# Kernel tuning notes

Measured on AMD Instinct MI355X. Metric: run time of the kernel, lower is better.

Reference implementation:

```python
import jax, jax.numpy as jnp
import numpy as np

B, T, S, C = 4096, 128, 16, 128
NEG = -1e30  # finite stand-in for -inf to keep grads NaN-free


def setup_inputs() -> dict:
    key = jax.random.key(0)
    k1, k2 = jax.random.split(key)
    prediction = jax.random.normal(k1, (B, T, C), dtype=jnp.float32)  # treated as log-probs, as in the original
    lable = jax.random.normal(k2, (B, S, C), dtype=jnp.float32)       # one-hot-ish label scores
    return {"prediction": prediction, "lable": lable}


def _ctc_nll(logp, targets):
    """CTC negative log-likelihood, full-length inputs/targets.
    logp: (B, T, C) log-probabilities, blank=0. targets: (B, S) int.
    Returns nll: (B,)."""
    Bb, Tt, Cc = logp.shape
    Ss = targets.shape[1]
    L = 2 * Ss + 1  # extended label: blank-interleaved
    neg = jnp.float32(NEG)

    ext = jnp.zeros((Bb, L), dtype=targets.dtype).at[:, 1::2].set(targets)
    # skip transition l-2 -> l allowed iff ext[l] != ext[l-2] (auto-false on blanks)
    skip_ok = jnp.concatenate(
        [jnp.zeros((Bb, 2), dtype=bool), ext[:, 2:] != ext[:, :-2]], axis=1)

    # gather log-probs of extended labels for every time step: (B, T, L)
    logp_ext = jnp.take_along_axis(logp, ext[:, None, :], axis=2)

    alpha0 = (jnp.full((Bb, L), neg)
              .at[:, 0].set(logp_ext[:, 0, 0])
              .at[:, 1].set(logp_ext[:, 0, 1]))

    pad1 = jnp.full((Bb, 1), neg)
    pad2 = jnp.full((Bb, 2), neg)

    def step(alpha, lp_t):
        a1 = alpha
        a2 = jnp.concatenate([pad1, alpha[:, :-1]], axis=1)
        a3 = jnp.where(skip_ok, jnp.concatenate([pad2, alpha[:, :-2]], axis=1), neg)
        alpha_new = jnp.logaddexp(jnp.logaddexp(a1, a2), a3) + lp_t
        return alpha_new, None

    alpha_T, _ = jax.lax.scan(step, alpha0, jnp.swapaxes(logp_ext, 0, 1)[1:])
    nll = -jnp.logaddexp(alpha_T[:, -1], alpha_T[:, -2])
    return nll


def reference(prediction, lable):
    # synthesize_lable: per-(b,s) argmax over classes -> integer targets (B, S)
    targets = jnp.argmax(lable, axis=-1)
    nll = _ctc_nll(prediction, targets)
    # zero_infinity=True
    nll = jnp.where(jnp.isfinite(nll), nll, jnp.float32(0.0))
    # reduction='mean': divide each loss by its target length, then batch-mean
    Ss = lable.shape[1]
    return jnp.mean(nll / jnp.float32(Ss))
```

## Files before the change

kernel.cpp:

```cpp
#include <hip/hip_runtime.h>
#include <math.h>
#include <stdint.h>

#define B_ 4096
#define T_ 128
#define S_ 16
#define C_ 128
#define L_ 33
#define NSLOT 17
#define NELEM (T_ * NSLOT)
#define NEGV (-1e30f)
#define LOG2E 1.4426950408889634f
#define LN2 0.6931471805599453f
#define NEGB (NEGV * LOG2E)

__device__ __forceinline__ float hexp2(float x) { return __builtin_amdgcn_exp2f(x); }
__device__ __forceinline__ float hlog2(float x) { return __builtin_amdgcn_logf(x); }

typedef const __attribute__((address_space(1))) unsigned int* gas_t;
typedef __attribute__((address_space(3))) unsigned int* las_t;

__global__ __launch_bounds__(256) void ctc_alpha_kernel(
        const float* __restrict__ pred,
        const float* __restrict__ lab,
        float* __restrict__ out_b) {
    const int wid  = threadIdx.x >> 6;
    const int lane = threadIdx.x & 63;
    const int b = blockIdx.x * 4 + wid;

    __shared__ int   cls_tab[4][NSLOT];
    __shared__ float lps[4][NELEM];

    const float* lrow = lab + (size_t)b * S_ * C_;
    float v0[S_], v1[S_];
    #pragma unroll
    for (int s = 0; s < S_; ++s) {
        v0[s] = lrow[s * C_ + lane];
        v1[s] = lrow[s * C_ + lane + 64];
    }
    if (lane == 0) cls_tab[wid][0] = 0;
    #pragma unroll
    for (int s = 0; s < S_; ++s) {
        float v; int idx;
        if (v1[s] > v0[s]) { v = v1[s]; idx = lane + 64; } else { v = v0[s]; idx = lane; }
        #pragma unroll
        for (int off = 32; off >= 1; off >>= 1) {
            float ov = __shfl_xor(v, off, 64);
            int   oi = __shfl_xor(idx, off, 64);
            if (ov > v || (ov == v && oi < idx)) { v = ov; idx = oi; }
        }
        if (lane == 0) cls_tab[wid][1 + s] = idx;
    }
    __syncthreads();

    const float* pb = pred + (size_t)b * T_ * C_;
    float* mylds = lps[wid];
    #pragma unroll
    for (int i = 0; i < NELEM / 64; ++i) {
        unsigned e = i * 64 + lane;
        unsigned t = e / NSLOT;
        unsigned s = e - t * NSLOT;
        int c = cls_tab[wid][s];
        const float* src = pb + (size_t)t * C_ + c;
        __builtin_amdgcn_global_load_lds((gas_t)src, (las_t)(mylds + i * 64), 4, 0, 0);
    }
    asm volatile("s_waitcnt vmcnt(0)" ::: "memory");

    const int l = lane;
    int cidx = 0;
    bool skipv = false;
    if (l < L_ && (l & 1)) {
        cidx = 1 + ((l - 1) >> 1);
        if (l >= 3) skipv = (cls_tab[wid][cidx] != cls_tab[wid][cidx - 1]);
    }
    const bool has2 = (l >= 1);

    float beta = (l <= 1) ? mylds[cidx] * LOG2E : NEGB;

    float lpA = mylds[1 * NSLOT + cidx];
    float lpB = mylds[2 * NSLOT + cidx];
    float lpC = mylds[3 * NSLOT + cidx];
    #pragma unroll 4
    for (int t = 1; t < T_; ++t) {
        float lp = lpA; lpA = lpB; lpB = lpC;
        if (t + 3 < T_) lpC = mylds[(t + 3) * NSLOT + cidx];
        float a2 = __shfl_up(beta, 1, 64);
        float a3 = __shfl_up(beta, 2, 64);
        a2 = has2  ? a2 : NEGB;
        a3 = skipv ? a3 : NEGB;
        float m = fmaxf(fmaxf(beta, a2), a3);
        float s = hexp2(beta - m) + hexp2(a2 - m) + hexp2(a3 - m);
        beta = fmaf(lp, LOG2E, m + hlog2(s));
    }

    float b31 = __shfl(beta, L_ - 2, 64);
    float b32 = __shfl(beta, L_ - 1, 64);
    if (lane == 0) {
        float m = fmaxf(b31, b32);
        float lse2 = m + hlog2(hexp2(b31 - m) + hexp2(b32 - m));
        float nll = -lse2 * LN2;
        if (!isfinite(nll)) nll = 0.0f;
        out_b[b] = nll * (1.0f / (float)S_);
    }
}

__global__ __launch_bounds__(256) void reduce_mean_kernel(
        const float* __restrict__ in, float* __restrict__ out) {
    __shared__ float sm[256];
    const int tid = threadIdx.x;
    float v[16];
    #pragma unroll
    for (int i = 0; i < 16; ++i) v[i] = in[tid + i * 256];
    float s = 0.f;
    #pragma unroll
    for (int i = 0; i < 16; ++i) s += v[i];
    sm[tid] = s;
    __syncthreads();
    for (int w = 128; w >= 1; w >>= 1) {
        if (tid < w) sm[tid] += sm[tid + w];
        __syncthreads();
    }
    if (tid == 0) out[0] = sm[0] / (float)B_;
}

extern "C" void kernel_launch(void* const* d_in, const int* in_sizes, int n_in,
                              void* d_out, int out_size, void* d_ws, size_t ws_size,
                              hipStream_t stream) {
    const float* pred = (const float*)d_in[0];
    const float* lab  = (const float*)d_in[1];
    float* ws = (float*)d_ws;
    ctc_alpha_kernel<<<B_ / 4, 256, 0, stream>>>(pred, lab, ws);
    reduce_mean_kernel<<<1, 256, 0, stream>>>(ws, (float*)d_out);
}
```

Measured before the change: 67.79 us.

## Overlap gathered log-prob loads with alpha recursion and pack argmax into 64-bit keys

Splits the async global-to-LDS gather so the recursion waits only for the first half of the loads (vmcnt(17)) and runs the first 60 time steps while the rest are still in flight. The label argmax now processes two label rows per wavefront half and packs value plus inverted index into a 64-bit key, which halves the shuffle reduction depth. The block barrier is replaced by a per-wave lgkmcnt wait. The LDS buffer is padded so the loop can prefetch past the end without a bounds check. Correctness depends on the vmcnt counting and the load ordering lining up with the split point, and on each wave's LDS writes being visible to its own lanes without a block barrier.

```diff
diff --git a/kernel.cpp b/kernel.cpp
--- a/kernel.cpp
+++ b/kernel.cpp
@@ -17,6 +17,11 @@
 __device__ __forceinline__ float hexp2(float x) { return __builtin_amdgcn_exp2f(x); }
 __device__ __forceinline__ float hlog2(float x) { return __builtin_amdgcn_logf(x); }
 
+__device__ __forceinline__ unsigned fkey(float v) {
+    unsigned u = __float_as_uint(v);
+    return (u & 0x80000000u) ? ~u : (u | 0x80000000u);
+}
+
 typedef const __attribute__((address_space(1))) unsigned int* gas_t;
 typedef __attribute__((address_space(3))) unsigned int* las_t;
 
@@ -29,34 +34,41 @@
     const int b = blockIdx.x * 4 + wid;
 
     __shared__ int   cls_tab[4][NSLOT];
-    __shared__ float lps[4][NELEM];
+    __shared__ float lps[4][NELEM + 64];
 
-    const float* lrow = lab + (size_t)b * S_ * C_;
-    float v0[S_], v1[S_];
+    const int half = lane >> 5;
+    const int li   = lane & 31;
+    const float* lrow = lab + (size_t)b * S_ * C_ + (size_t)half * C_ + li;
+    float vv[8][4];
     #pragma unroll
-    for (int s = 0; s < S_; ++s) {
-        v0[s] = lrow[s * C_ + lane];
-        v1[s] = lrow[s * C_ + lane + 64];
-    }
+    for (int sp = 0; sp < 8; ++sp)
+        #pragma unroll
+        for (int k = 0; k < 4; ++k)
+            vv[sp][k] = lrow[(size_t)sp * 2 * C_ + k * 32];
+
     if (lane == 0) cls_tab[wid][0] = 0;
     #pragma unroll
-    for (int s = 0; s < S_; ++s) {
-        float v; int idx;
-        if (v1[s] > v0[s]) { v = v1[s]; idx = lane + 64; } else { v = v0[s]; idx = lane; }
+    for (int sp = 0; sp < 8; ++sp) {
+        unsigned long long key = 0;
         #pragma unroll
-        for (int off = 32; off >= 1; off >>= 1) {
-            float ov = __shfl_xor(v, off, 64);
-            int   oi = __shfl_xor(idx, off, 64);
-            if (ov > v || (ov == v && oi < idx)) { v = ov; idx = oi; }
+        for (int k = 0; k < 4; ++k) {
+            unsigned long long kk =
+                ((unsigned long long)fkey(vv[sp][k]) << 32) | (unsigned)(~(li + 32 * k));
+            if (kk > key) key = kk;
         }
-        if (lane == 0) cls_tab[wid][1 + s] = idx;
+        #pragma unroll
+        for (int off = 16; off >= 1; off >>= 1) {
+            unsigned long long ok = __shfl_xor(key, off, 64);
+            if (ok > key) key = ok;
+        }
+        if (li == 0) cls_tab[wid][1 + sp * 2 + half] = (int)(~(unsigned)key) & 127;
     }
-    __syncthreads();
+    asm volatile("s_waitcnt lgkmcnt(0)" ::: "memory");
 
     const float* pb = pred + (size_t)b * T_ * C_;
     float* mylds = lps[wid];
     #pragma unroll
-    for (int i = 0; i < NELEM / 64; ++i) {
+    for (int i = 0; i < 34; ++i) {
         unsigned e = i * 64 + lane;
         unsigned t = e / NSLOT;
         unsigned s = e - t * NSLOT;
@@ -64,7 +76,6 @@
         const float* src = pb + (size_t)t * C_ + c;
         __builtin_amdgcn_global_load_lds((gas_t)src, (las_t)(mylds + i * 64), 4, 0, 0);
     }
-    asm volatile("s_waitcnt vmcnt(0)" ::: "memory");
 
     const int l = lane;
     int cidx = 0;
@@ -75,15 +86,32 @@
     }
     const bool has2 = (l >= 1);
 
+    asm volatile("s_waitcnt vmcnt(17)" ::: "memory");
+
     float beta = (l <= 1) ? mylds[cidx] * LOG2E : NEGB;
-
     float lpA = mylds[1 * NSLOT + cidx];
     float lpB = mylds[2 * NSLOT + cidx];
     float lpC = mylds[3 * NSLOT + cidx];
+
     #pragma unroll 4
-    for (int t = 1; t < T_; ++t) {
+    for (int t = 1; t <= 60; ++t) {
         float lp = lpA; lpA = lpB; lpB = lpC;
-        if (t + 3 < T_) lpC = mylds[(t + 3) * NSLOT + cidx];
+        lpC = mylds[(t + 3) * NSLOT + cidx];
+        float a2 = __shfl_up(beta, 1, 64);
+        float a3 = __shfl_up(beta, 2, 64);
+        a2 = has2  ? a2 : NEGB;
+        a3 = skipv ? a3 : NEGB;
+        float m = fmaxf(fmaxf(beta, a2), a3);
+        float s = hexp2(beta - m) + hexp2(a2 - m) + hexp2(a3 - m);
+        beta = fmaf(lp, LOG2E, m + hlog2(s));
+    }
+
+    asm volatile("s_waitcnt vmcnt(0)" ::: "memory");
+
+    #pragma unroll 4
+    for (int t = 61; t < T_; ++t) {
+        float lp = lpA; lpA = lpB; lpB = lpC;
+        lpC = mylds[(t + 3) * NSLOT + cidx];
         float a2 = __shfl_up(beta, 1, 64);
         float a3 = __shfl_up(beta, 2, 64);
         a2 = has2  ? a2 : NEGB;
```

Measured after the change: 63.10 us. -6.9%, faster.
